# Optimization experiments

Measured on AMD Instinct MI355X. Metric: run time of the kernel, lower is better.

Reference implementation:

```python
import jax, jax.numpy as jnp
import numpy as np

N, E = 100000, 1600000
IN_DIM, HID, OUT, L = 64, 64, 10, 3
BN_EPS = 1e-5

def _bn(x, g, b):
    # BatchNorm1d training-mode forward: biased variance over the node axis
    m = jnp.mean(x, axis=0)
    v = jnp.var(x, axis=0)
    return (x - m) * jax.lax.rsqrt(v + BN_EPS) * g + b

def setup_inputs() -> dict:
    key = jax.random.key(0)
    ks = jax.random.split(key, 16)
    s_in = 1.0 / np.sqrt(IN_DIM)
    s_h = 1.0 / np.sqrt(HID)
    s_c = 1.0 / np.sqrt(HID * (L + 1))
    return {
        "x": jax.random.normal(ks[0], (N, IN_DIM), jnp.float32),
        "edge_index": jax.random.randint(ks[1], (2, E), 0, N, jnp.int32),
        "W_in": jax.random.uniform(ks[2], (IN_DIM, HID), jnp.float32, -s_in, s_in),
        "b_in": jnp.zeros((HID,), jnp.float32),
        "g_in": jnp.ones((HID,), jnp.float32),
        "be_in": jnp.zeros((HID,), jnp.float32),
        "eps": jnp.full((L,), 0.1, jnp.float32),
        "W1": jax.random.uniform(ks[3], (L, HID, HID), jnp.float32, -s_h, s_h),
        "b1": jnp.zeros((L, HID), jnp.float32),
        "g1": jnp.ones((L, HID), jnp.float32),
        "be1": jnp.zeros((L, HID), jnp.float32),
        "W2": jax.random.uniform(ks[4], (L, HID, HID), jnp.float32, -s_h, s_h),
        "b2": jnp.zeros((L, HID), jnp.float32),
        "g2": jnp.ones((L, HID), jnp.float32),
        "be2": jnp.zeros((L, HID), jnp.float32),
        "g_post": jnp.ones((L, HID), jnp.float32),
        "be_post": jnp.zeros((L, HID), jnp.float32),
        "W_out1": jax.random.uniform(ks[5], (HID * (L + 1), HID), jnp.float32, -s_c, s_c),
        "b_out1": jnp.zeros((HID,), jnp.float32),
        "g_out": jnp.ones((HID,), jnp.float32),
        "be_out": jnp.zeros((HID,), jnp.float32),
        "W_out2": jax.random.uniform(ks[6], (HID, OUT), jnp.float32, -s_h, s_h),
        "b_out2": jnp.zeros((OUT,), jnp.float32),
    }

def reference(x, edge_index, W_in, b_in, g_in, be_in, eps, W1, b1, g1, be1,
              W2, b2, g2, be2, g_post, be_post, W_out1, b_out1, g_out, be_out,
              W_out2, b_out2):
    src, dst = edge_index[0], edge_index[1]
    # input projection (dropout is identity in eval)
    h = jax.nn.relu(_bn(x @ W_in + b_in, g_in, be_in))
    layer_outputs = [h]
    for i in range(L):
        # GIN aggregation: gather neighbor feats, scatter-add to dst
        aggr = jax.ops.segment_sum(h[src], dst, num_segments=N)  # (N, HID)
        o = (1.0 + eps[i]) * h + aggr
        o = jax.nn.relu(_bn(o @ W1[i] + b1[i], g1[i], be1[i]))
        o = jax.nn.relu(_bn(o @ W2[i] + b2[i], g2[i], be2[i]))
        h = jax.nn.relu(_bn(o, g_post[i], be_post[i]))
        layer_outputs.append(h)
    h = jnp.concatenate(layer_outputs, axis=-1)  # (N, 4*HID)
    h = jax.nn.relu(_bn(h @ W_out1 + b_out1, g_out, be_out))
    return h @ W_out2 + b_out2
```

## Files before the change

### kernel.cpp

```cpp
#include <hip/hip_runtime.h>


#define HID 64
#define LAYERS 3
#define BN_EPS 1e-5f

#define BK_SHIFT 8
#define BK_MAX 512
#define PART_EPT 16

__device__ __forceinline__ float relu_aff(float x, float s, float t) {
    return fmaxf(fmaf(x, s, t), 0.f);
}

__device__ __forceinline__ void bn_fin(const float* __restrict__ raw, const float* __restrict__ g,
                                       const float* __restrict__ b, float invN, int c,
                                       float& s, float& t) {
    float m = raw[c] * invN;
    float v = fmaf(-m, m, raw[64 + c] * invN);
    float r = rsqrtf(v + BN_EPS);
    s = r * g[c];
    t = fmaf(-m, s, b[c]);
}


__global__ __launch_bounds__(256) void k_bhist(const int* __restrict__ dst, int* __restrict__ gh,
                                               int E, int nbk) {
    __shared__ int h[BK_MAX];
    for (int i = threadIdx.x; i < BK_MAX; i += 256) h[i] = 0;
    __syncthreads();
    int stride = gridDim.x * 256;
    for (int e = blockIdx.x * 256 + threadIdx.x; e < E; e += stride)
        atomicAdd(&h[dst[e] >> BK_SHIFT], 1);
    __syncthreads();
    for (int i = threadIdx.x; i < nbk; i += 256)
        if (h[i]) atomicAdd(&gh[i], h[i]);
}

__global__ __launch_bounds__(512) void k_bscan(const int* __restrict__ gh, int* __restrict__ boff,
                                               int* __restrict__ gcur, int nbk) {
    int lane = threadIdx.x & 63, wid = threadIdx.x >> 6;
    int v = (threadIdx.x < nbk) ? gh[threadIdx.x] : 0;
    int incl = v;
    for (int d = 1; d < 64; d <<= 1) { int y = __shfl_up(incl, d); if (lane >= d) incl += y; }
    __shared__ int ws[8];
    if (lane == 63) ws[wid] = incl;
    __syncthreads();
    if (threadIdx.x == 0) { int a = 0; for (int w = 0; w < 8; w++) { int t = ws[w]; ws[w] = a; a += t; } }
    __syncthreads();
    int excl = incl - v + ws[wid];
    if (threadIdx.x < nbk) { boff[threadIdx.x] = excl; gcur[threadIdx.x] = excl; }
    if (threadIdx.x == nbk - 1) boff[nbk] = excl + v;
}

__global__ __launch_bounds__(256) void k_bpart(const int* __restrict__ src, const int* __restrict__ dst,
                                               int* __restrict__ gcur, unsigned* __restrict__ pairs,
                                               int E) {
    __shared__ int h[BK_MAX], cur[BK_MAX], base[BK_MAX];
    int e0 = blockIdx.x * (256 * PART_EPT);
    int eend = min(e0 + 256 * PART_EPT, E);
    for (int i = threadIdx.x; i < BK_MAX; i += 256) h[i] = 0;
    __syncthreads();
    for (int e = e0 + threadIdx.x; e < eend; e += 256)
        atomicAdd(&h[dst[e] >> BK_SHIFT], 1);
    __syncthreads();
    for (int i = threadIdx.x; i < BK_MAX; i += 256) {
        cur[i] = 0;
        base[i] = h[i] ? atomicAdd(&gcur[i], h[i]) : 0;
    }
    __syncthreads();
    for (int e = e0 + threadIdx.x; e < eend; e += 256) {
        int d = dst[e];
        int b = d >> BK_SHIFT;
        int r = atomicAdd(&cur[b], 1);
        pairs[base[b] + r] = ((unsigned)(d & ((1 << BK_SHIFT) - 1)) << 24) | (unsigned)src[e];
    }
}

__global__ __launch_bounds__(256) void k_bucket_csr(const unsigned* __restrict__ pairs,
                                                    const int* __restrict__ boff,
                                                    int* __restrict__ row_off, int* __restrict__ col,
                                                    int N, int E, int nbk) {
    int b = blockIdx.x;
    int p0 = boff[b], p1 = boff[b + 1];
    int base_node = b << BK_SHIFT;
    int nn = min(256, N - base_node);
    __shared__ int h[256], cur[256];
    h[threadIdx.x] = 0;
    __syncthreads();
    for (int p = p0 + threadIdx.x; p < p1; p += 256)
        atomicAdd(&h[pairs[p] >> 24], 1);
    __syncthreads();
    int v = h[threadIdx.x];
    int lane = threadIdx.x & 63, wid = threadIdx.x >> 6;
    int incl = v;
    for (int d = 1; d < 64; d <<= 1) { int y = __shfl_up(incl, d); if (lane >= d) incl += y; }
    __shared__ int ws[4];
    if (lane == 63) ws[wid] = incl;
    __syncthreads();
    if (threadIdx.x == 0) { int a = 0; for (int w = 0; w < 4; w++) { int t = ws[w]; ws[w] = a; a += t; } }
    __syncthreads();
    int excl = incl - v + ws[wid];
    if (threadIdx.x < nn) row_off[base_node + threadIdx.x] = p0 + excl;
    if (b == nbk - 1 && threadIdx.x == 0) row_off[N] = E;
    cur[threadIdx.x] = excl;
    __syncthreads();
    for (int p = p0 + threadIdx.x; p < p1; p += 256) {
        unsigned pk = pairs[p];
        int local = pk >> 24;
        int r = atomicAdd(&cur[local], 1);
        col[p0 + r] = (int)(pk & 0xFFFFFFu);
    }
}

__global__ __launch_bounds__(256) void k_redstats(const float* __restrict__ pst,
                                                  float* __restrict__ rawOut, int nblk) {
    int slot = blockIdx.x * 4 + (threadIdx.x >> 6);
    int lane = threadIdx.x & 63;
    float s = 0.f;
    for (int b = lane; b < nblk; b += 64) s += pst[(size_t)b * 128 + slot];
#pragma unroll
    for (int m = 1; m < 64; m <<= 1) s += __shfl_xor(s, m, 64);
    if (lane == 0) rawOut[slot] = s;
}

__global__ __launch_bounds__(256) void k_agg(const float* __restrict__ hb,
                                             const float* __restrict__ raw, const float* __restrict__ g,
                                             const float* __restrict__ b, float invN,
                                             const int* __restrict__ row_off, const int* __restrict__ col,
                                             const float* __restrict__ epsp, int li,
                                             float* __restrict__ o, int n) {
    int wid = threadIdx.x >> 6, lane = threadIdx.x & 63;
    int node = blockIdx.x * 4 + wid;
    if (node >= n) return;
    int sub = lane >> 4;
    int fc = (lane & 15) * 4;
    float s0, t0, s1, t1, s2, t2, s3, t3;
    bn_fin(raw, g, b, invN, fc + 0, s0, t0);
    bn_fin(raw, g, b, invN, fc + 1, s1, t1);
    bn_fin(raw, g, b, invN, fc + 2, s2, t2);
    bn_fin(raw, g, b, invN, fc + 3, s3, t3);
    float ax = 0.f, ay = 0.f, az = 0.f, aw = 0.f;
    int e = row_off[node], e1 = row_off[node + 1];

    while (e + 16 <= e1) {
        int i0 = col[e + sub], i1 = col[e + 4 + sub], i2 = col[e + 8 + sub], i3 = col[e + 12 + sub];
        float4 v0 = *(const float4*)&hb[(size_t)i0 * HID + fc];
        float4 v1 = *(const float4*)&hb[(size_t)i1 * HID + fc];
        float4 v2 = *(const float4*)&hb[(size_t)i2 * HID + fc];
        float4 v3 = *(const float4*)&hb[(size_t)i3 * HID + fc];
        ax += relu_aff(v0.x, s0, t0) + relu_aff(v1.x, s0, t0) + relu_aff(v2.x, s0, t0) + relu_aff(v3.x, s0, t0);
        ay += relu_aff(v0.y, s1, t1) + relu_aff(v1.y, s1, t1) + relu_aff(v2.y, s1, t1) + relu_aff(v3.y, s1, t1);
        az += relu_aff(v0.z, s2, t2) + relu_aff(v1.z, s2, t2) + relu_aff(v2.z, s2, t2) + relu_aff(v3.z, s2, t2);
        aw += relu_aff(v0.w, s3, t3) + relu_aff(v1.w, s3, t3) + relu_aff(v2.w, s3, t3) + relu_aff(v3.w, s3, t3);
        e += 16;
    }
    while (e + 4 <= e1) {
        int i = col[e + sub];
        float4 v = *(const float4*)&hb[(size_t)i * HID + fc];
        ax += relu_aff(v.x, s0, t0);
        ay += relu_aff(v.y, s1, t1);
        az += relu_aff(v.z, s2, t2);
        aw += relu_aff(v.w, s3, t3);
        e += 4;
    }
    int rem = e1 - e;
    if (sub < rem) {
        int i = col[e + sub];
        float4 v = *(const float4*)&hb[(size_t)i * HID + fc];
        ax += relu_aff(v.x, s0, t0);
        ay += relu_aff(v.y, s1, t1);
        az += relu_aff(v.z, s2, t2);
        aw += relu_aff(v.w, s3, t3);
    }
    ax += __shfl_xor(ax, 16, 64); ay += __shfl_xor(ay, 16, 64);
    az += __shfl_xor(az, 16, 64); aw += __shfl_xor(aw, 16, 64);
    ax += __shfl_xor(ax, 32, 64); ay += __shfl_xor(ay, 32, 64);
    az += __shfl_xor(az, 32, 64); aw += __shfl_xor(aw, 32, 64);
    if (sub == 0) {
        float ope = 1.f + epsp[li];
        float4 h4 = *(const float4*)&hb[(size_t)node * HID + fc];
        float4 r;
        r.x = fmaf(ope, relu_aff(h4.x, s0, t0), ax);
        r.y = fmaf(ope, relu_aff(h4.y, s1, t1), ay);
        r.z = fmaf(ope, relu_aff(h4.z, s2, t2), az);
        r.w = fmaf(ope, relu_aff(h4.w, s3, t3), aw);
        *(float4*)&o[(size_t)node * HID + fc] = r;
    }
}

template <bool AFF, bool STATS>
__global__ __launch_bounds__(256) void k_gemm_t64(const float* __restrict__ A,
                                                  const float* __restrict__ raw, const float* __restrict__ g,
                                                  const float* __restrict__ b, float invN,
                                                  const float* __restrict__ W, const float* __restrict__ bias,
                                                  float* __restrict__ C, float* __restrict__ pst, int n) {
    __shared__ float stl[2 * HID];
    __shared__ float sA[64 * HID];
    __shared__ float ps[4][64], pq[4][64];
    if (AFF) {
        if (threadIdx.x < HID) {
            float s, t;
            bn_fin(raw, g, b, invN, threadIdx.x, s, t);
            stl[threadIdx.x] = s;
            stl[HID + threadIdx.x] = t;
        }
        __syncthreads();
    }
    int base = blockIdx.x * 64;
#pragma unroll
    for (int it = 0; it < 4; it++) {
        int idx4 = it * 256 + threadIdx.x;
        int r = idx4 >> 4;
        int kc = (idx4 & 15) * 4;
        float4 v = make_float4(0.f, 0.f, 0.f, 0.f);
        if (base + r < n) {
            v = *(const float4*)&A[(size_t)(base + r) * HID + kc];
            if (AFF) {
                v.x = relu_aff(v.x, stl[kc + 0], stl[HID + kc + 0]);
                v.y = relu_aff(v.y, stl[kc + 1], stl[HID + kc + 1]);
                v.z = relu_aff(v.z, stl[kc + 2], stl[HID + kc + 2]);
                v.w = relu_aff(v.w, stl[kc + 3], stl[HID + kc + 3]);
            }
        }
        *(float4*)&sA[idx4 * 4] = v;
    }
    __syncthreads();

    int lane = threadIdx.x & 63;
    int wv = threadIdx.x >> 6;
    int r0 = __builtin_amdgcn_readfirstlane(wv * 16);
    float acc[16];
#pragma unroll
    for (int r = 0; r < 16; r++) acc[r] = 0.f;
    const float* Wl = W + lane;
#pragma unroll 4
    for (int kk = 0; kk < 16; kk++) {
        float w0 = Wl[(4 * kk + 0) * HID];
        float w1 = Wl[(4 * kk + 1) * HID];
        float w2 = Wl[(4 * kk + 2) * HID];
        float w3 = Wl[(4 * kk + 3) * HID];
#pragma unroll
        for (int r = 0; r < 16; r++) {
            const float4 av = *(const float4*)&sA[(r0 + r) * HID + 4 * kk];
            acc[r] = fmaf(av.x, w0, acc[r]);
            acc[r] = fmaf(av.y, w1, acc[r]);
            acc[r] = fmaf(av.z, w2, acc[r]);
            acc[r] = fmaf(av.w, w3, acc[r]);
        }
    }
    float bsl = bias[lane];
    float ssum = 0.f, ssq = 0.f;
#pragma unroll
    for (int r = 0; r < 16; r++) {
        int row = base + r0 + r;
        if (row < n) {
            float v = acc[r] + bsl;
            C[(size_t)row * HID + lane] = v;
            if (STATS) { ssum += v; ssq = fmaf(v, v, ssq); }
        }
    }
    if (STATS) {
        ps[wv][lane] = ssum;
        pq[wv][lane] = ssq;
        __syncthreads();
        if (threadIdx.x < 64) {
            float s = ps[0][threadIdx.x] + ps[1][threadIdx.x] + ps[2][threadIdx.x] + ps[3][threadIdx.x];
            float q = pq[0][threadIdx.x] + pq[1][threadIdx.x] + pq[2][threadIdx.x] + pq[3][threadIdx.x];
            pst[(size_t)blockIdx.x * 128 + threadIdx.x] = s;
            pst[(size_t)blockIdx.x * 128 + 64 + threadIdx.x] = q;
        }
    }
}

__global__ __launch_bounds__(256) void k_gemm_out1_t(const float* __restrict__ B0, const float* __restrict__ B1,
                                                     const float* __restrict__ B2, const float* __restrict__ B3,
                                                     const float* __restrict__ R0, const float* __restrict__ R1,
                                                     const float* __restrict__ R2, const float* __restrict__ R3,
                                                     const float* __restrict__ G0, const float* __restrict__ G1,
                                                     const float* __restrict__ G2, const float* __restrict__ G3,
                                                     const float* __restrict__ E0, const float* __restrict__ E1,
                                                     const float* __restrict__ E2, const float* __restrict__ E3,
                                                     float invN,
                                                     const float* __restrict__ W, const float* __restrict__ bias,
                                                     float* __restrict__ C, float* __restrict__ pst, int n) {
    __shared__ float stl[4][2 * HID];
    __shared__ float sA[64 * HID];
    __shared__ float ps[4][64], pq[4][64];
    {
        int p = threadIdx.x >> 6, c = threadIdx.x & 63;
        const float* rp[4] = {R0, R1, R2, R3};
        const float* gp[4] = {G0, G1, G2, G3};
        const float* ep[4] = {E0, E1, E2, E3};
        float s, t;
        bn_fin(rp[p], gp[p], ep[p], invN, c, s, t);
        stl[p][c] = s;
        stl[p][HID + c] = t;
    }
    __syncthreads();

    int base = blockIdx.x * 64;
    int lane = threadIdx.x & 63;
    int wv = threadIdx.x >> 6;
    int r0 = __builtin_amdgcn_readfirstlane(wv * 16);
    float acc[16];
#pragma unroll
    for (int r = 0; r < 16; r++) acc[r] = 0.f;
    const float* bufs[4] = {B0, B1, B2, B3};
#pragma unroll
    for (int pp = 0; pp < 4; pp++) {
        if (pp) __syncthreads();
        const float* Bp = bufs[pp];
#pragma unroll
        for (int it = 0; it < 4; it++) {
            int idx4 = it * 256 + threadIdx.x;
            int r = idx4 >> 4;
            int kc = (idx4 & 15) * 4;
            float4 v = make_float4(0.f, 0.f, 0.f, 0.f);
            if (base + r < n) {
                v = *(const float4*)&Bp[(size_t)(base + r) * HID + kc];
                v.x = relu_aff(v.x, stl[pp][kc + 0], stl[pp][HID + kc + 0]);
                v.y = relu_aff(v.y, stl[pp][kc + 1], stl[pp][HID + kc + 1]);
                v.z = relu_aff(v.z, stl[pp][kc + 2], stl[pp][HID + kc + 2]);
                v.w = relu_aff(v.w, stl[pp][kc + 3], stl[pp][HID + kc + 3]);
            }
            *(float4*)&sA[idx4 * 4] = v;
        }
        __syncthreads();
        const float* Wl = W + (size_t)pp * HID * HID + lane;
#pragma unroll 4
        for (int kk = 0; kk < 16; kk++) {
            float w0 = Wl[(4 * kk + 0) * HID];
            float w1 = Wl[(4 * kk + 1) * HID];
            float w2 = Wl[(4 * kk + 2) * HID];
            float w3 = Wl[(4 * kk + 3) * HID];
#pragma unroll
            for (int r = 0; r < 16; r++) {
                const float4 av = *(const float4*)&sA[(r0 + r) * HID + 4 * kk];
                acc[r] = fmaf(av.x, w0, acc[r]);
                acc[r] = fmaf(av.y, w1, acc[r]);
                acc[r] = fmaf(av.z, w2, acc[r]);
                acc[r] = fmaf(av.w, w3, acc[r]);
            }
        }
    }
    float bsl = bias[lane];
    float ssum = 0.f, ssq = 0.f;
#pragma unroll
    for (int r = 0; r < 16; r++) {
        int row = base + r0 + r;
        if (row < n) {
            float v = acc[r] + bsl;
            C[(size_t)row * HID + lane] = v;
            ssum += v; ssq = fmaf(v, v, ssq);
        }
    }
    ps[wv][lane] = ssum;
    pq[wv][lane] = ssq;
    __syncthreads();
    if (threadIdx.x < 64) {
        float s = ps[0][threadIdx.x] + ps[1][threadIdx.x] + ps[2][threadIdx.x] + ps[3][threadIdx.x];
        float q = pq[0][threadIdx.x] + pq[1][threadIdx.x] + pq[2][threadIdx.x] + pq[3][threadIdx.x];
        pst[(size_t)blockIdx.x * 128 + threadIdx.x] = s;
        pst[(size_t)blockIdx.x * 128 + 64 + threadIdx.x] = q;
    }
}

__global__ __launch_bounds__(256) void k_gemm_out2_t(const float* __restrict__ A,
                                                     const float* __restrict__ raw, const float* __restrict__ g,
                                                     const float* __restrict__ b, float invN,
                                                     const float* __restrict__ W, const float* __restrict__ bias,
                                                     float* __restrict__ C, int n) {
    __shared__ float stl[2 * HID];
    if (threadIdx.x < HID) {
        float s, t;
        bn_fin(raw, g, b, invN, threadIdx.x, s, t);
        stl[threadIdx.x] = s;
        stl[HID + threadIdx.x] = t;
    }
    __syncthreads();
    int lane = threadIdx.x & 63;
    int wv = threadIdx.x >> 6;
    int k0 = __builtin_amdgcn_readfirstlane(wv * 16);
    int row = blockIdx.x * 64 + lane;
    bool valid = row < n;
    float acc[10];
#pragma unroll
    for (int j = 0; j < 10; j++) acc[j] = 0.f;
    if (valid) {
        const float4* a4 = (const float4*)(A + (size_t)row * HID + k0);
#pragma unroll
        for (int kk = 0; kk < 4; kk++) {
            float4 av = a4[kk];
            float a[4] = {av.x, av.y, av.z, av.w};
#pragma unroll
            for (int u = 0; u < 4; u++) {
                int k = k0 + kk * 4 + u;
                float xv = relu_aff(a[u], stl[k], stl[HID + k]);
#pragma unroll
                for (int j = 0; j < 10; j++) acc[j] = fmaf(xv, W[k * 10 + j], acc[j]);
            }
        }
    }
    __shared__ float part[4][64][10];
#pragma unroll
    for (int j = 0; j < 10; j++) part[wv][lane][j] = acc[j];
    __syncthreads();
    if (wv == 0 && valid) {
        float* cp = C + (size_t)row * 10;
#pragma unroll
        for (int j = 0; j < 10; j++)
            cp[j] = bias[j] + part[0][lane][j] + part[1][lane][j] + part[2][lane][j] + part[3][lane][j];
    }
}

__global__ __launch_bounds__(256) void k_affine_stats(float* __restrict__ X,
                                                      const float* __restrict__ rawIn,
                                                      const float* __restrict__ g, const float* __restrict__ b,
                                                      float invN,
                                                      float* __restrict__ pst, long long n64) {
    long long stride = (long long)gridDim.x * 256;
    long long i0 = (long long)blockIdx.x * 256 + threadIdx.x;
    int col = threadIdx.x & 63;
    float sA, tA;
    bn_fin(rawIn, g, b, invN, col, sA, tA);
    float s = 0.f, q = 0.f;
    for (long long i = i0; i < n64; i += stride) {
        float v = relu_aff(X[i], sA, tA);
        X[i] = v;
        s += v; q = fmaf(v, v, q);
    }
    __shared__ float ls[256], lq[256];
    ls[threadIdx.x] = s; lq[threadIdx.x] = q;
    __syncthreads();
    if (threadIdx.x < 64) {
        s = ls[threadIdx.x] + ls[threadIdx.x + 64] + ls[threadIdx.x + 128] + ls[threadIdx.x + 192];
        q = lq[threadIdx.x] + lq[threadIdx.x + 64] + lq[threadIdx.x + 128] + lq[threadIdx.x + 192];
        pst[(size_t)blockIdx.x * 128 + col] = s;
        pst[(size_t)blockIdx.x * 128 + 64 + col] = q;
    }
}

extern "C" void kernel_launch(void* const* d_in, const int* in_sizes, int n_in,
                              void* d_out, int out_size, void* d_ws, size_t ws_size,
                              hipStream_t stream) {
    const float* x = (const float*)d_in[0];
    const int* ei = (const int*)d_in[1];
    const float* W_in = (const float*)d_in[2];
    const float* b_in = (const float*)d_in[3];
    const float* g_in = (const float*)d_in[4];
    const float* be_in = (const float*)d_in[5];
    const float* epsp = (const float*)d_in[6];
    const float* W1 = (const float*)d_in[7];
    const float* b1 = (const float*)d_in[8];
    const float* g1 = (const float*)d_in[9];
    const float* be1 = (const float*)d_in[10];
    const float* W2 = (const float*)d_in[11];
    const float* b2 = (const float*)d_in[12];
    const float* g2 = (const float*)d_in[13];
    const float* be2 = (const float*)d_in[14];
    const float* g_post = (const float*)d_in[15];
    const float* be_post = (const float*)d_in[16];
    const float* W_out1 = (const float*)d_in[17];
    const float* b_out1 = (const float*)d_in[18];
    const float* g_out = (const float*)d_in[19];
    const float* be_out = (const float*)d_in[20];
    const float* W_out2 = (const float*)d_in[21];
    const float* b_out2 = (const float*)d_in[22];

    const int N = in_sizes[0] / HID;
    const int E = in_sizes[1] / 2;
    const int* srcp = ei;
    const int* dstp = ei + E;

    const int nbk = (N + (1 << BK_SHIFT) - 1) >> BK_SHIFT;
    if (nbk > BK_MAX) return;
    if (N > (1 << 24)) return;

    size_t NODE = (size_t)N * HID;
    float* f = (float*)d_ws;
    float* pre0 = f;
    float* z0 = f + NODE;
    float* z1 = f + 2 * NODE;
    float* z2 = f + 3 * NODE;
    float* o = f + 4 * NODE;
    float* p = f + 5 * NODE;
    int* rc = (int*)(f + 6 * NODE);
    int* col = rc + (N + 1);
    int* gh = col + E;
    int* boff = gh + 512;
    int* gcur = boff + 513;
    float* raw = (float*)(gcur + 512);
    unsigned* pairs = (unsigned*)o;

    size_t need = (size_t)(6 * NODE) * 4 + ((size_t)(N + 1) + E + 1537) * 4 + (size_t)11 * 128 * 4;
    if (ws_size < need) return;

    float invN = 1.0f / (float)N;
    int gt = (N + 63) / 64;
    int pb = (E + 256 * PART_EPT - 1) / (256 * PART_EPT);

    hipMemsetAsync(gh, 0, 512 * sizeof(int), stream);

    k_bhist<<<512, 256, 0, stream>>>(dstp, gh, E, nbk);
    k_bscan<<<1, 512, 0, stream>>>(gh, boff, gcur, nbk);
    k_bpart<<<pb, 256, 0, stream>>>(srcp, dstp, gcur, pairs, E);
    k_bucket_csr<<<nbk, 256, 0, stream>>>(pairs, boff, rc, col, N, E, nbk);

    k_gemm_t64<false, true><<<gt, 256, 0, stream>>>(x, nullptr, nullptr, nullptr, invN,
                                                    W_in, b_in, pre0, o, N);
    k_redstats<<<32, 256, 0, stream>>>(o, raw, gt);

    float* zb[3] = {z0, z1, z2};
    for (int i = 0; i < LAYERS; i++) {
        int s1 = 1 + 3 * i, s2 = 2 + 3 * i, sp = 3 + 3 * i;
        const float* hb = (i == 0) ? pre0 : zb[i - 1];
        const float* rh = (i == 0) ? raw : raw + (size_t)(3 * i) * 128;
        const float* gh2 = (i == 0) ? g_in : g_post + (i - 1) * HID;
        const float* eh = (i == 0) ? be_in : be_post + (i - 1) * HID;
        k_agg<<<(N + 3) / 4, 256, 0, stream>>>(hb, rh, gh2, eh, invN, rc, col, epsp, i, o, N);
        k_gemm_t64<false, true><<<gt, 256, 0, stream>>>(o, nullptr, nullptr, nullptr, invN,
                                                        W1 + (size_t)i * HID * HID, b1 + i * HID,
                                                        p, zb[i], N);
        k_redstats<<<32, 256, 0, stream>>>(zb[i], raw + (size_t)s1 * 128, gt);
        k_gemm_t64<true, true><<<gt, 256, 0, stream>>>(p, raw + (size_t)s1 * 128, g1 + i * HID, be1 + i * HID,
                                                       invN, W2 + (size_t)i * HID * HID, b2 + i * HID,
                                                       zb[i], o, N);
        k_redstats<<<32, 256, 0, stream>>>(o, raw + (size_t)s2 * 128, gt);
        k_affine_stats<<<512, 256, 0, stream>>>(zb[i], raw + (size_t)s2 * 128, g2 + i * HID, be2 + i * HID, invN,
                                                o, (long long)NODE);
        k_redstats<<<32, 256, 0, stream>>>(o, raw + (size_t)sp * 128, 512);
    }

    k_gemm_out1_t<<<gt, 256, 0, stream>>>(pre0, z0, z1, z2,
                                          raw, raw + 3 * 128, raw + 6 * 128, raw + 9 * 128,
                                          g_in, g_post, g_post + HID, g_post + 2 * HID,
                                          be_in, be_post, be_post + HID, be_post + 2 * HID,
                                          invN, W_out1, b_out1, p, o, N);
    k_redstats<<<32, 256, 0, stream>>>(o, raw + 10 * 128, gt);
    k_gemm_out2_t<<<gt, 256, 0, stream>>>(p, raw + 10 * 128, g_out, be_out, invN,
                                          W_out2, b_out2, (float*)d_out, N);
}
```

Before: 795.9 us.

## Use 4x4 register tiles with transposed A and LDS-staged weights in GEMMs

The 64-wide GEMM kernels change from one output column and 16 rows per thread to a 4x4 register tile per thread. A is stored transposed in shared memory with a padded stride of 65, and W is copied into shared memory, so each k step does two float4 LDS reads for 16 FMAs. Before, each k step read W from global memory and did 16 LDS reads. Column statistics are now reduced with cross-lane shuffles before the block-level sum. The costs are extra LDS traffic to stage W in every block, and float4 reads at the stride-65 transposed layout that are not 16-byte aligned.

```diff
diff --git a/kernel.cpp b/kernel.cpp
--- a/kernel.cpp
+++ b/kernel.cpp
@@ -189,6 +189,22 @@
     }
 }
 
+
+#define GEMM44_COMPUTE(sAT, sW, acc, r0, c0)                                \
+    _Pragma("unroll 8")                                                     \
+    for (int k = 0; k < HID; k++) {                                         \
+        float4 a = *(const float4*)&sAT[k * 65 + r0];                       \
+        float4 w = *(const float4*)&sW[k * HID + c0];                       \
+        acc[0]  = fmaf(a.x, w.x, acc[0]);  acc[1]  = fmaf(a.x, w.y, acc[1]);\
+        acc[2]  = fmaf(a.x, w.z, acc[2]);  acc[3]  = fmaf(a.x, w.w, acc[3]);\
+        acc[4]  = fmaf(a.y, w.x, acc[4]);  acc[5]  = fmaf(a.y, w.y, acc[5]);\
+        acc[6]  = fmaf(a.y, w.z, acc[6]);  acc[7]  = fmaf(a.y, w.w, acc[7]);\
+        acc[8]  = fmaf(a.z, w.x, acc[8]);  acc[9]  = fmaf(a.z, w.y, acc[9]);\
+        acc[10] = fmaf(a.z, w.z, acc[10]); acc[11] = fmaf(a.z, w.w, acc[11]);\
+        acc[12] = fmaf(a.w, w.x, acc[12]); acc[13] = fmaf(a.w, w.y, acc[13]);\
+        acc[14] = fmaf(a.w, w.z, acc[14]); acc[15] = fmaf(a.w, w.w, acc[15]);\
+    }
+
 template <bool AFF, bool STATS>
 __global__ __launch_bounds__(256) void k_gemm_t64(const float* __restrict__ A,
                                                   const float* __restrict__ raw, const float* __restrict__ g,
@@ -196,8 +212,9 @@
                                                   const float* __restrict__ W, const float* __restrict__ bias,
                                                   float* __restrict__ C, float* __restrict__ pst, int n) {
     __shared__ float stl[2 * HID];
-    __shared__ float sA[64 * HID];
-    __shared__ float ps[4][64], pq[4][64];
+    __shared__ float sAT[HID * 65];
+    __shared__ float sW[HID * HID];
+    __shared__ float ps[4][HID], pq[4][HID];
     if (AFF) {
         if (threadIdx.x < HID) {
             float s, t;
@@ -210,9 +227,14 @@
     int base = blockIdx.x * 64;
 #pragma unroll
     for (int it = 0; it < 4; it++) {
-        int idx4 = it * 256 + threadIdx.x;
-        int r = idx4 >> 4;
-        int kc = (idx4 & 15) * 4;
+        int idx = it * 256 + threadIdx.x;
+        *(float4*)&sW[idx * 4] = *(const float4*)&W[idx * 4];
+    }
+#pragma unroll
+    for (int it = 0; it < 4; it++) {
+        int idx = it * 256 + threadIdx.x;
+        int r = idx >> 4;
+        int kc = (idx & 15) * 4;
         float4 v = make_float4(0.f, 0.f, 0.f, 0.f);
         if (base + r < n) {
             v = *(const float4*)&A[(size_t)(base + r) * HID + kc];
@@ -223,46 +245,55 @@
                 v.w = relu_aff(v.w, stl[kc + 3], stl[HID + kc + 3]);
             }
         }
-        *(float4*)&sA[idx4 * 4] = v;
-    }
-    __syncthreads();
-
-    int lane = threadIdx.x & 63;
-    int wv = threadIdx.x >> 6;
-    int r0 = __builtin_amdgcn_readfirstlane(wv * 16);
+        sAT[(kc + 0) * 65 + r] = v.x;
+        sAT[(kc + 1) * 65 + r] = v.y;
+        sAT[(kc + 2) * 65 + r] = v.z;
+        sAT[(kc + 3) * 65 + r] = v.w;
+    }
+    __syncthreads();
+
+    int c0 = (threadIdx.x & 15) * 4;
+    int r0 = (threadIdx.x >> 4) * 4;
     float acc[16];
 #pragma unroll
-    for (int r = 0; r < 16; r++) acc[r] = 0.f;
-    const float* Wl = W + lane;
-#pragma unroll 4
-    for (int kk = 0; kk < 16; kk++) {
-        float w0 = Wl[(4 * kk + 0) * HID];
-        float w1 = Wl[(4 * kk + 1) * HID];
-        float w2 = Wl[(4 * kk + 2) * HID];
-        float w3 = Wl[(4 * kk + 3) * HID];
-#pragma unroll
-        for (int r = 0; r < 16; r++) {
-            const float4 av = *(const float4*)&sA[(r0 + r) * HID + 4 * kk];
-            acc[r] = fmaf(av.x, w0, acc[r]);
-            acc[r] = fmaf(av.y, w1, acc[r]);
-            acc[r] = fmaf(av.z, w2, acc[r]);
-            acc[r] = fmaf(av.w, w3, acc[r]);
-        }
-    }
-    float bsl = bias[lane];
-    float ssum = 0.f, ssq = 0.f;
-#pragma unroll
-    for (int r = 0; r < 16; r++) {
-        int row = base + r0 + r;
+    for (int j = 0; j < 16; j++) acc[j] = 0.f;
+    GEMM44_COMPUTE(sAT, sW, acc, r0, c0)
+
+    float4 bs = *(const float4*)&bias[c0];
+    float sc0 = 0.f, sc1 = 0.f, sc2 = 0.f, sc3 = 0.f;
+    float qc0 = 0.f, qc1 = 0.f, qc2 = 0.f, qc3 = 0.f;
+#pragma unroll
+    for (int ri = 0; ri < 4; ri++) {
+        int row = base + r0 + ri;
         if (row < n) {
-            float v = acc[r] + bsl;
-            C[(size_t)row * HID + lane] = v;
-            if (STATS) { ssum += v; ssq = fmaf(v, v, ssq); }
+            float4 v;
+            v.x = acc[ri * 4 + 0] + bs.x;
+            v.y = acc[ri * 4 + 1] + bs.y;
+            v.z = acc[ri * 4 + 2] + bs.z;
+            v.w = acc[ri * 4 + 3] + bs.w;
+            *(float4*)&C[(size_t)row * HID + c0] = v;
+            if (STATS) {
+                sc0 += v.x; qc0 = fmaf(v.x, v.x, qc0);
+                sc1 += v.y; qc1 = fmaf(v.y, v.y, qc1);
+                sc2 += v.z; qc2 = fmaf(v.z, v.z, qc2);
+                sc3 += v.w; qc3 = fmaf(v.w, v.w, qc3);
+            }
         }
     }
     if (STATS) {
-        ps[wv][lane] = ssum;
-        pq[wv][lane] = ssq;
+        int lane = threadIdx.x & 63, wv = threadIdx.x >> 6;
+        sc0 += __shfl_xor(sc0, 16, 64); sc0 += __shfl_xor(sc0, 32, 64);
+        sc1 += __shfl_xor(sc1, 16, 64); sc1 += __shfl_xor(sc1, 32, 64);
+        sc2 += __shfl_xor(sc2, 16, 64); sc2 += __shfl_xor(sc2, 32, 64);
+        sc3 += __shfl_xor(sc3, 16, 64); sc3 += __shfl_xor(sc3, 32, 64);
+        qc0 += __shfl_xor(qc0, 16, 64); qc0 += __shfl_xor(qc0, 32, 64);
+        qc1 += __shfl_xor(qc1, 16, 64); qc1 += __shfl_xor(qc1, 32, 64);
+        qc2 += __shfl_xor(qc2, 16, 64); qc2 += __shfl_xor(qc2, 32, 64);
+        qc3 += __shfl_xor(qc3, 16, 64); qc3 += __shfl_xor(qc3, 32, 64);
+        if (lane < 16) {
+            *(float4*)&ps[wv][c0] = make_float4(sc0, sc1, sc2, sc3);
+            *(float4*)&pq[wv][c0] = make_float4(qc0, qc1, qc2, qc3);
+        }
         __syncthreads();
         if (threadIdx.x < 64) {
             float s = ps[0][threadIdx.x] + ps[1][threadIdx.x] + ps[2][threadIdx.x] + ps[3][threadIdx.x];
@@ -285,8 +316,9 @@
                                                      const float* __restrict__ W, const float* __restrict__ bias,
                                                      float* __restrict__ C, float* __restrict__ pst, int n) {
     __shared__ float stl[4][2 * HID];
-    __shared__ float sA[64 * HID];
-    __shared__ float ps[4][64], pq[4][64];
+    __shared__ float sAT[HID * 65];
+    __shared__ float sW[HID * HID];
+    __shared__ float ps[4][HID], pq[4][HID];
     {
         int p = threadIdx.x >> 6, c = threadIdx.x & 63;
         const float* rp[4] = {R0, R1, R2, R3};
@@ -300,22 +332,27 @@
     __syncthreads();
 
     int base = blockIdx.x * 64;
-    int lane = threadIdx.x & 63;
-    int wv = threadIdx.x >> 6;
-    int r0 = __builtin_amdgcn_readfirstlane(wv * 16);
+    int c0 = (threadIdx.x & 15) * 4;
+    int r0 = (threadIdx.x >> 4) * 4;
     float acc[16];
 #pragma unroll
-    for (int r = 0; r < 16; r++) acc[r] = 0.f;
+    for (int j = 0; j < 16; j++) acc[j] = 0.f;
     const float* bufs[4] = {B0, B1, B2, B3};
 #pragma unroll
     for (int pp = 0; pp < 4; pp++) {
         if (pp) __syncthreads();
         const float* Bp = bufs[pp];
+        const float* Wp = W + (size_t)pp * HID * HID;
 #pragma unroll
         for (int it = 0; it < 4; it++) {
-            int idx4 = it * 256 + threadIdx.x;
-            int r = idx4 >> 4;
-            int kc = (idx4 & 15) * 4;
+            int idx = it * 256 + threadIdx.x;
+            *(float4*)&sW[idx * 4] = *(const float4*)&Wp[idx * 4];
+        }
+#pragma unroll
+        for (int it = 0; it < 4; it++) {
+            int idx = it * 256 + threadIdx.x;
+            int r = idx >> 4;
+            int kc = (idx & 15) * 4;
             float4 v = make_float4(0.f, 0.f, 0.f, 0.f);
             if (base + r < n) {
                 v = *(const float4*)&Bp[(size_t)(base + r) * HID + kc];
@@ -324,39 +361,47 @@
                 v.z = relu_aff(v.z, stl[pp][kc + 2], stl[pp][HID + kc + 2]);
                 v.w = relu_aff(v.w, stl[pp][kc + 3], stl[pp][HID + kc + 3]);
             }
-            *(float4*)&sA[idx4 * 4] = v;
+            sAT[(kc + 0) * 65 + r] = v.x;
+            sAT[(kc + 1) * 65 + r] = v.y;
+            sAT[(kc + 2) * 65 + r] = v.z;
+            sAT[(kc + 3) * 65 + r] = v.w;
         }
         __syncthreads();
-        const float* Wl = W + (size_t)pp * HID * HID + lane;
-#pragma unroll 4
-        for (int kk = 0; kk < 16; kk++) {
-            float w0 = Wl[(4 * kk + 0) * HID];
-            float w1 = Wl[(4 * kk + 1) * HID];
-            float w2 = Wl[(4 * kk + 2) * HID];
-            float w3 = Wl[(4 * kk + 3) * HID];
-#pragma unroll
-            for (int r = 0; r < 16; r++) {
-                const float4 av = *(const float4*)&sA[(r0 + r) * HID + 4 * kk];
-                acc[r] = fmaf(av.x, w0, acc[r]);
-                acc[r] = fmaf(av.y, w1, acc[r]);
-                acc[r] = fmaf(av.z, w2, acc[r]);
-                acc[r] = fmaf(av.w, w3, acc[r]);
-            }
-        }
-    }
-    float bsl = bias[lane];
-    float ssum = 0.f, ssq = 0.f;
-#pragma unroll
-    for (int r = 0; r < 16; r++) {
-        int row = base + r0 + r;
+        GEMM44_COMPUTE(sAT, sW, acc, r0, c0)
+    }
+
+    float4 bs = *(const float4*)&bias[c0];
+    float sc0 = 0.f, sc1 = 0.f, sc2 = 0.f, sc3 = 0.f;
+    float qc0 = 0.f, qc1 = 0.f, qc2 = 0.f, qc3 = 0.f;
+#pragma unroll
+    for (int ri = 0; ri < 4; ri++) {
+        int row = base + r0 + ri;
         if (row < n) {
-            float v = acc[r] + bsl;
-            C[(size_t)row * HID + lane] = v;
-            ssum += v; ssq = fmaf(v, v, ssq);
-        }
-    }
-    ps[wv][lane] = ssum;
-    pq[wv][lane] = ssq;
+            float4 v;
+            v.x = acc[ri * 4 + 0] + bs.x;
+            v.y = acc[ri * 4 + 1] + bs.y;
+            v.z = acc[ri * 4 + 2] + bs.z;
+            v.w = acc[ri * 4 + 3] + bs.w;
+            *(float4*)&C[(size_t)row * HID + c0] = v;
+            sc0 += v.x; qc0 = fmaf(v.x, v.x, qc0);
+            sc1 += v.y; qc1 = fmaf(v.y, v.y, qc1);
+            sc2 += v.z; qc2 = fmaf(v.z, v.z, qc2);
+            sc3 += v.w; qc3 = fmaf(v.w, v.w, qc3);
+        }
+    }
+    int lane = threadIdx.x & 63, wv = threadIdx.x >> 6;
+    sc0 += __shfl_xor(sc0, 16, 64); sc0 += __shfl_xor(sc0, 32, 64);
+    sc1 += __shfl_xor(sc1, 16, 64); sc1 += __shfl_xor(sc1, 32, 64);
+    sc2 += __shfl_xor(sc2, 16, 64); sc2 += __shfl_xor(sc2, 32, 64);
+    sc3 += __shfl_xor(sc3, 16, 64); sc3 += __shfl_xor(sc3, 32, 64);
+    qc0 += __shfl_xor(qc0, 16, 64); qc0 += __shfl_xor(qc0, 32, 64);
+    qc1 += __shfl_xor(qc1, 16, 64); qc1 += __shfl_xor(qc1, 32, 64);
+    qc2 += __shfl_xor(qc2, 16, 64); qc2 += __shfl_xor(qc2, 32, 64);
+    qc3 += __shfl_xor(qc3, 16, 64); qc3 += __shfl_xor(qc3, 32, 64);
+    if (lane < 16) {
+        *(float4*)&ps[wv][c0] = make_float4(sc0, sc1, sc2, sc3);
+        *(float4*)&pq[wv][c0] = make_float4(qc0, qc1, qc2, qc3);
+    }
     __syncthreads();
     if (threadIdx.x < 64) {
         float s = ps[0][threadIdx.x] + ps[1][threadIdx.x] + ps[2][threadIdx.x] + ps[3][threadIdx.x];
```

Result: faster. 721.5 us (-9.3%).

## Remap GEMM tiles so each lane owns a row and scalar-load weights

Applied to the files above, without the earlier changes.

The 64-wide GEMM kernels now give each lane one row and each wave 16 output columns, instead of each lane owning one column across 16 rows. The A tile is stored in LDS with stride 65 to avoid bank conflicts on per-lane row reads. Weight reads become wave-uniform, so they can be scalar loads. Outputs are written as float4 per row. BN column statistics are now reduced with wave shuffles instead of an LDS cross-wave reduction. In exchange, the shuffle reduction costs 16×6×2 shuffles per wave, and the LDS stores become scalar.

```diff
diff --git a/kernel.cpp b/kernel.cpp
--- a/kernel.cpp
+++ b/kernel.cpp
@@ -189,6 +189,18 @@
     }
 }
 
+__device__ __forceinline__ void gemm_rows64(const float* __restrict__ sA,
+                                            const float* __restrict__ Wbase,
+                                            int lane, int c0, float acc[16]) {
+#pragma unroll 4
+    for (int k = 0; k < HID; k++) {
+        float a = sA[lane * 65 + k];
+        const float* wr = Wbase + k * HID + c0;
+#pragma unroll
+        for (int j = 0; j < 16; j++) acc[j] = fmaf(a, wr[j], acc[j]);
+    }
+}
+
 template <bool AFF, bool STATS>
 __global__ __launch_bounds__(256) void k_gemm_t64(const float* __restrict__ A,
                                                   const float* __restrict__ raw, const float* __restrict__ g,
@@ -196,8 +208,7 @@
                                                   const float* __restrict__ W, const float* __restrict__ bias,
                                                   float* __restrict__ C, float* __restrict__ pst, int n) {
     __shared__ float stl[2 * HID];
-    __shared__ float sA[64 * HID];
-    __shared__ float ps[4][64], pq[4][64];
+    __shared__ float sA[64 * 65];
     if (AFF) {
         if (threadIdx.x < HID) {
             float s, t;
@@ -210,9 +221,9 @@
     int base = blockIdx.x * 64;
 #pragma unroll
     for (int it = 0; it < 4; it++) {
-        int idx4 = it * 256 + threadIdx.x;
-        int r = idx4 >> 4;
-        int kc = (idx4 & 15) * 4;
+        int idx = it * 256 + threadIdx.x;
+        int r = idx >> 4;
+        int kc = (idx & 15) * 4;
         float4 v = make_float4(0.f, 0.f, 0.f, 0.f);
         if (base + r < n) {
             v = *(const float4*)&A[(size_t)(base + r) * HID + kc];
@@ -223,52 +234,44 @@
                 v.w = relu_aff(v.w, stl[kc + 3], stl[HID + kc + 3]);
             }
         }
-        *(float4*)&sA[idx4 * 4] = v;
+        sA[r * 65 + kc + 0] = v.x;
+        sA[r * 65 + kc + 1] = v.y;
+        sA[r * 65 + kc + 2] = v.z;
+        sA[r * 65 + kc + 3] = v.w;
     }
     __syncthreads();
 
     int lane = threadIdx.x & 63;
-    int wv = threadIdx.x >> 6;
-    int r0 = __builtin_amdgcn_readfirstlane(wv * 16);
+    int c0 = __builtin_amdgcn_readfirstlane((threadIdx.x >> 6) * 16);
+    int row = base + lane;
+    bool valid = row < n;
     float acc[16];
 #pragma unroll
-    for (int r = 0; r < 16; r++) acc[r] = 0.f;
-    const float* Wl = W + lane;
-#pragma unroll 4
-    for (int kk = 0; kk < 16; kk++) {
-        float w0 = Wl[(4 * kk + 0) * HID];
-        float w1 = Wl[(4 * kk + 1) * HID];
-        float w2 = Wl[(4 * kk + 2) * HID];
-        float w3 = Wl[(4 * kk + 3) * HID];
-#pragma unroll
-        for (int r = 0; r < 16; r++) {
-            const float4 av = *(const float4*)&sA[(r0 + r) * HID + 4 * kk];
-            acc[r] = fmaf(av.x, w0, acc[r]);
-            acc[r] = fmaf(av.y, w1, acc[r]);
-            acc[r] = fmaf(av.z, w2, acc[r]);
-            acc[r] = fmaf(av.w, w3, acc[r]);
+    for (int j = 0; j < 16; j++) acc[j] = 0.f;
+    gemm_rows64(sA, W, lane, c0, acc);
+
+    float v[16];
+#pragma unroll
+    for (int j = 0; j < 16; j++) v[j] = valid ? acc[j] + bias[c0 + j] : 0.f;
+    if (valid) {
+        float4* cp = (float4*)(C + (size_t)row * HID + c0);
+#pragma unroll
+        for (int u = 0; u < 4; u++)
+            cp[u] = make_float4(v[4 * u], v[4 * u + 1], v[4 * u + 2], v[4 * u + 3]);
+    }
+    if (STATS) {
+        float mysum = 0.f, mysq = 0.f;
+#pragma unroll
+        for (int j = 0; j < 16; j++) {
+            float s = v[j];
+            float q = s * s;
+#pragma unroll
+            for (int m = 1; m < 64; m <<= 1) { s += __shfl_xor(s, m, 64); q += __shfl_xor(q, m, 64); }
+            if (lane == j) { mysum = s; mysq = q; }
         }
-    }
-    float bsl = bias[lane];
-    float ssum = 0.f, ssq = 0.f;
-#pragma unroll
-    for (int r = 0; r < 16; r++) {
-        int row = base + r0 + r;
-        if (row < n) {
-            float v = acc[r] + bsl;
-            C[(size_t)row * HID + lane] = v;
-            if (STATS) { ssum += v; ssq = fmaf(v, v, ssq); }
-        }
-    }
-    if (STATS) {
-        ps[wv][lane] = ssum;
-        pq[wv][lane] = ssq;
-        __syncthreads();
-        if (threadIdx.x < 64) {
-            float s = ps[0][threadIdx.x] + ps[1][threadIdx.x] + ps[2][threadIdx.x] + ps[3][threadIdx.x];
-            float q = pq[0][threadIdx.x] + pq[1][threadIdx.x] + pq[2][threadIdx.x] + pq[3][threadIdx.x];
-            pst[(size_t)blockIdx.x * 128 + threadIdx.x] = s;
-            pst[(size_t)blockIdx.x * 128 + 64 + threadIdx.x] = q;
+        if (lane < 16) {
+            pst[(size_t)blockIdx.x * 128 + c0 + lane] = mysum;
+            pst[(size_t)blockIdx.x * 128 + 64 + c0 + lane] = mysq;
         }
     }
 }
@@ -285,8 +288,7 @@
                                                      const float* __restrict__ W, const float* __restrict__ bias,
                                                      float* __restrict__ C, float* __restrict__ pst, int n) {
     __shared__ float stl[4][2 * HID];
-    __shared__ float sA[64 * HID];
-    __shared__ float ps[4][64], pq[4][64];
+    __shared__ float sA[64 * 65];
     {
         int p = threadIdx.x >> 6, c = threadIdx.x & 63;
         const float* rp[4] = {R0, R1, R2, R3};
@@ -301,11 +303,12 @@
 
     int base = blockIdx.x * 64;
     int lane = threadIdx.x & 63;
-    int wv = threadIdx.x >> 6;
-    int r0 = __builtin_amdgcn_readfirstlane(wv * 16);
+    int c0 = __builtin_amdgcn_readfirstlane((threadIdx.x >> 6) * 16);
+    int row = base + lane;
+    bool valid = row < n;
     float acc[16];
 #pragma unroll
-    for (int r = 0; r < 16; r++) acc[r] = 0.f;
+    for (int j = 0; j < 16; j++) acc[j] = 0.f;
     const float* bufs[4] = {B0, B1, B2, B3};
 #pragma unroll
     for (int pp = 0; pp < 4; pp++) {
@@ -313,56 +316,47 @@
         const float* Bp = bufs[pp];
 #pragma unroll
         for (int it = 0; it < 4; it++) {
-            int idx4 = it * 256 + threadIdx.x;
-            int r = idx4 >> 4;
-            int kc = (idx4 & 15) * 4;
-            float4 v = make_float4(0.f, 0.f, 0.f, 0.f);
+            int idx = it * 256 + threadIdx.x;
+            int r = idx >> 4;
+            int kc = (idx & 15) * 4;
+            float4 vv = make_float4(0.f, 0.f, 0.f, 0.f);
             if (base + r < n) {
-                v = *(const float4*)&Bp[(size_t)(base + r) * HID + kc];
-                v.x = relu_aff(v.x, stl[pp][kc + 0], stl[pp][HID + kc + 0]);
-                v.y = relu_aff(v.y, stl[pp][kc + 1], stl[pp][HID + kc + 1]);
-                v.z = relu_aff(v.z, stl[pp][kc + 2], stl[pp][HID + kc + 2]);
-                v.w = relu_aff(v.w, stl[pp][kc + 3], stl[pp][HID + kc + 3]);
+                vv = *(const float4*)&Bp[(size_t)(base + r) * HID + kc];
+                vv.x = relu_aff(vv.x, stl[pp][kc + 0], stl[pp][HID + kc + 0]);
+                vv.y = relu_aff(vv.y, stl[pp][kc + 1], stl[pp][HID + kc + 1]);
+                vv.z = relu_aff(vv.z, stl[pp][kc + 2], stl[pp][HID + kc + 2]);
+                vv.w = relu_aff(vv.w, stl[pp][kc + 3], stl[pp][HID + kc + 3]);
             }
-            *(float4*)&sA[idx4 * 4] = v;
+            sA[r * 65 + kc + 0] = vv.x;
+            sA[r * 65 + kc + 1] = vv.y;
+            sA[r * 65 + kc + 2] = vv.z;
+            sA[r * 65 + kc + 3] = vv.w;
         }
         __syncthreads();
-        const float* Wl = W + (size_t)pp * HID * HID + lane;
-#pragma unroll 4
-        for (int kk = 0; kk < 16; kk++) {
-            float w0 = Wl[(4 * kk + 0) * HID];
-            float w1 = Wl[(4 * kk + 1) * HID];
-            float w2 = Wl[(4 * kk + 2) * HID];
-            float w3 = Wl[(4 * kk + 3) * HID];
-#pragma unroll
-            for (int r = 0; r < 16; r++) {
-                const float4 av = *(const float4*)&sA[(r0 + r) * HID + 4 * kk];
-                acc[r] = fmaf(av.x, w0, acc[r]);
-                acc[r] = fmaf(av.y, w1, acc[r]);
-                acc[r] = fmaf(av.z, w2, acc[r]);
-                acc[r] = fmaf(av.w, w3, acc[r]);
-            }
-        }
-    }
-    float bsl = bias[lane];
-    float ssum = 0.f, ssq = 0.f;
-#pragma unroll
-    for (int r = 0; r < 16; r++) {
-        int row = base + r0 + r;
-        if (row < n) {
-            float v = acc[r] + bsl;
-            C[(size_t)row * HID + lane] = v;
-            ssum += v; ssq = fmaf(v, v, ssq);
-        }
-    }
-    ps[wv][lane] = ssum;
-    pq[wv][lane] = ssq;
-    __syncthreads();
-    if (threadIdx.x < 64) {
-        float s = ps[0][threadIdx.x] + ps[1][threadIdx.x] + ps[2][threadIdx.x] + ps[3][threadIdx.x];
-        float q = pq[0][threadIdx.x] + pq[1][threadIdx.x] + pq[2][threadIdx.x] + pq[3][threadIdx.x];
-        pst[(size_t)blockIdx.x * 128 + threadIdx.x] = s;
-        pst[(size_t)blockIdx.x * 128 + 64 + threadIdx.x] = q;
+        gemm_rows64(sA, W + (size_t)pp * HID * HID, lane, c0, acc);
+    }
+
+    float v[16];
+#pragma unroll
+    for (int j = 0; j < 16; j++) v[j] = valid ? acc[j] + bias[c0 + j] : 0.f;
+    if (valid) {
+        float4* cp = (float4*)(C + (size_t)row * HID + c0);
+#pragma unroll
+        for (int u = 0; u < 4; u++)
+            cp[u] = make_float4(v[4 * u], v[4 * u + 1], v[4 * u + 2], v[4 * u + 3]);
+    }
+    float mysum = 0.f, mysq = 0.f;
+#pragma unroll
+    for (int j = 0; j < 16; j++) {
+        float s = v[j];
+        float q = s * s;
+#pragma unroll
+        for (int m = 1; m < 64; m <<= 1) { s += __shfl_xor(s, m, 64); q += __shfl_xor(q, m, 64); }
+        if (lane == j) { mysum = s; mysq = q; }
+    }
+    if (lane < 16) {
+        pst[(size_t)blockIdx.x * 128 + c0 + lane] = mysum;
+        pst[(size_t)blockIdx.x * 128 + 64 + c0 + lane] = mysq;
     }
 }
 
```

New measurement: 794.5 us. No clear change (-0.2%).
